# Kernel optimization log

Hardware: AMD Instinct MI355X
Metric: run time of the kernel (lower is better)

## Reference

```python
import jax, jax.numpy as jnp
import numpy as np

KH = KW = 3
SH = SW = 1
PH = PW = 1


def _im2col(x, kh, kw, sh, sw, ph, pw):
    # x: [N, C, H, W] -> cols: [N, C*kh*kw, H_out*W_out], ordering (C, kh, kw)
    N, C, H, W = x.shape
    H_out = (H + 2 * ph - kh) // sh + 1
    W_out = (W + 2 * pw - kw) // sw + 1
    x_pad = jnp.pad(x, ((0, 0), (0, 0), (ph, ph), (pw, pw)))
    # fixed small loop over kernel offsets (kh*kw = 9), strided slices
    patches = [x_pad[:, :, i:i + sh * H_out:sh, j:j + sw * W_out:sw]
               for i in range(kh) for j in range(kw)]  # each [N, C, H_out, W_out]
    cols = jnp.stack(patches, axis=2)  # [N, C, kh*kw, H_out, W_out]
    cols = cols.reshape(N, C * kh * kw, H_out * W_out)
    return cols, H_out, W_out


def setup_inputs() -> dict:
    key = jax.random.key(0)
    k1, k2, k3 = jax.random.split(key, 3)
    x = jax.random.normal(k1, (16, 128, 56, 56), dtype=jnp.float32)
    weight = jax.random.normal(k2, (256, 128, 3, 3), dtype=jnp.float32) * 0.05
    fan_in = 128 * 3 * 3
    bound = 1.0 / fan_in ** 0.5
    bias = jax.random.uniform(k3, (256,), dtype=jnp.float32, minval=-bound, maxval=bound)
    return {"x": x, "weight": weight, "bias": bias}


def reference(x, weight, bias):
    # im2col unfold + (analog) matmul conv; noise_cfg=None -> plain matmul
    cols, H_out, W_out = _im2col(x, KH, KW, SH, SW, PH, PW)  # [N, K, L]
    N = cols.shape[0]
    Cout = weight.shape[0]
    Wmat = weight.reshape(Cout, -1)  # [Cout, K], K = C*kh*kw
    # y[n, l, o] = sum_k cols[n, k, l] * Wmat[o, k]  (AnalogMatMulFn without noise)
    y = jnp.einsum('nkl,ok->nol', cols, Wmat)  # [N, Cout, L]
    y = y.reshape(N, Cout, H_out, W_out)
    y = y + bias[None, :, None, None]
    return y
```

## Files before the change

### kernel.cpp

```cpp
#include <hip/hip_runtime.h>
#include <hip/hip_bf16.h>
#include <stdint.h>


typedef __attribute__((ext_vector_type(8))) short short8;
typedef __attribute__((ext_vector_type(4))) float floatx4;

__device__ static inline void gload_lds16(const void* g, void* l) {
  typedef const __attribute__((address_space(1))) unsigned int* gp_t;
  typedef __attribute__((address_space(3))) unsigned int* lp_t;
  __builtin_amdgcn_global_load_lds((gp_t)(uintptr_t)g, (lp_t)(uint32_t)(uintptr_t)l,
                                   16, 0, 0);
}

__global__ __launch_bounds__(256)
void pre_kernel(const float* __restrict__ x, const float* __restrict__ wsrc,
                __hip_bfloat16* __restrict__ xp, __hip_bfloat16* __restrict__ wt) {
  const int b = blockIdx.x;
  if (b < 16 * 58) {
    const int n = b / 58, hp = b % 58;
    __hip_bfloat16* dst = xp + (size_t)(n * 58 + hp) * 58 * 128;
    if (hp == 0 || hp == 57) {
      const uint4 z = {0, 0, 0, 0};
      uint4* p = (uint4*)dst;
      for (int i = threadIdx.x; i < 928; i += 256) p[i] = z;
      return;
    }
    const int h = hp - 1;
    __shared__ float tile[128][57];
    const float* src = x + (size_t)n * (128 * 3136) + h * 56;
    for (int i = threadIdx.x; i < 128 * 14; i += 256) {
      const int c = i / 14, q = i - c * 14;
      const float4 v = ((const float4*)(src + (size_t)c * 3136))[q];
      tile[c][4 * q + 0] = v.x;
      tile[c][4 * q + 1] = v.y;
      tile[c][4 * q + 2] = v.z;
      tile[c][4 * q + 3] = v.w;
    }
    __syncthreads();
    if (threadIdx.x < 32) {
      const uint4 z = {0, 0, 0, 0};
      const int col = (threadIdx.x >> 4) * 57;
      ((uint4*)(dst + (size_t)col * 128))[threadIdx.x & 15] = z;
    }
    __hip_bfloat16* di = dst + 128;
    for (int i = threadIdx.x; i < 56 * 16; i += 256) {
      const int w = i >> 4, c8 = (i & 15) * 8;
      union { uint4 u; __hip_bfloat16 hh[8]; } pk;
#pragma unroll
      for (int j = 0; j < 8; ++j) pk.hh[j] = __float2bfloat16(tile[c8 + j][w]);
      *(uint4*)(di + (size_t)w * 128 + c8) = pk.u;
    }
  } else {
    const int base = (b - 928) * 256 + threadIdx.x;
    for (int t = base; t < 256 * 9 * 128; t += 36 * 256) {
      const int e = t & 7;
      const int rr = (t >> 3) & 15;
      const int q = (t >> 7) & 3;
      const int ks = (t >> 9) & 1;
      const int ch = (t >> 10) & 1;
      const int t11 = t >> 11;
      const int kq = t11 % 9;
      const int g = t11 / 9;
      const int cout = g * 16 + rr;
      const int c = ch * 64 + ks * 32 + q * 8 + e;
      wt[t] = __float2bfloat16(wsrc[(size_t)(cout * 128 + c) * 9 + kq]);
    }
  }
}

#define STAGE(PH, BUF)                                                        \
  {                                                                           \
    const char* _src = pbase + (PH) * (58 * 256);                             \
    _Pragma("unroll") for (int _i = 0; _i < 4; ++_i) {                        \
      const int _j = _i * 256 + tid;                                          \
      const int _row = _j >> 4;                                               \
      const int _slot = _j & 15;                                              \
      gload_lds16(_src + _row * 256 + ((_slot ^ (_row & 7)) << 4),            \
                  (BUF) + _i * 4096 + wave * 1024);                           \
    }                                                                         \
    if (wave == 0) {                                                          \
      const int _j = 1024 + lane;                                             \
      const int _row = _j >> 4;                                               \
      const int _slot = _j & 15;                                              \
      gload_lds16(_src + _row * 256 + ((_slot ^ (_row & 7)) << 4),            \
                  (BUF) + 16384);                                             \
    }                                                                         \
  }

#define COMPUTE(P, BUF)                                                       \
  _Pragma("clang loop unroll(disable)") for (int _t = 0; _t < 12; ++_t) {     \
    const int _kw = _t >> 2;                                                  \
    const int _ksl = _t & 3;                                                  \
    const int _ofs = (P) * 3 * 4096 + _kw * 4096 + _ksl * 1024;               \
    _Pragma("unroll") for (int _mt = 0; _mt < 4; ++_mt)                       \
        areg[_mt] = *(const short8*)(pAw + _mt * 36864 + _ofs);               \
    _Pragma("unroll") for (int _nt = 0; _nt < 4; ++_nt) {                     \
      const int _rowL = rbase[_nt] + _kw;                                     \
      const int _pos = (_ksl * 4 + quad) ^ (_rowL & 7);                       \
      bfr[_nt] = *(const short8*)((BUF) + _rowL * 256 + (_pos << 4));         \
    }                                                                         \
    _Pragma("unroll") for (int _mt = 0; _mt < 4; ++_mt)                       \
        _Pragma("unroll") for (int _nt = 0; _nt < 4; ++_nt)                   \
            acc[_mt][_nt] = __builtin_amdgcn_mfma_f32_16x16x32_bf16(          \
                areg[_mt], bfr[_nt], acc[_mt][_nt], 0, 0, 0);                 \
  }

__global__ __launch_bounds__(256, 4)
void conv_gemm_kernel(const __hip_bfloat16* __restrict__ xp,
                      const __hip_bfloat16* __restrict__ wt,
                      const float* __restrict__ bias,
                      float* __restrict__ out) {
  __shared__ __align__(16) char smem[2][17408];

  const int tid = threadIdx.x;
  const int lane = tid & 63;
  const int wave = tid >> 6;
  const int col = lane & 15;
  const int quad = lane >> 4;

  const int id = blockIdx.x;
  const int xcd = id & 7;
  const int nt_ = xcd * 98 + (id >> 3);
  const int n0 = nt_ * 64;

  const int nimg0 = n0 / 3136;
  const int rem0 = n0 - nimg0 * 3136;
  const int hh0 = rem0 / 56;
  const int ww0 = rem0 - hh0 * 56;
  const int P0 = (nimg0 * 58 + hh0) * 58 + ww0;
  const char* pbase = (const char*)xp + (size_t)P0 * 256;

  STAGE(0, smem[0]);

  const char* pAw = (const char*)wt + (size_t)(wave * 4) * 36864 + lane * 16;

  int rbase[4];
#pragma unroll
  for (int nt = 0; nt < 4; ++nt) {
    const int pix = n0 + nt * 16 + col;
    const int ni = pix / 3136;
    const int re = pix - ni * 3136;
    const int ph = re / 56;
    const int pw = re - ph * 56;
    rbase[nt] = (ni * 58 + ph) * 58 + pw - P0;
  }

  floatx4 acc[4][4];
#pragma unroll
  for (int a = 0; a < 4; ++a)
#pragma unroll
    for (int c = 0; c < 4; ++c) acc[a][c] = (floatx4)0.f;

  short8 areg[4], bfr[4];

  __syncthreads();
  STAGE(1, smem[1]);
  COMPUTE(0, smem[0]);
  __syncthreads();
  STAGE(2, smem[0]);
  COMPUTE(1, smem[1]);
  __syncthreads();
  COMPUTE(2, smem[0]);

  const int rb = quad * 4;
#pragma unroll
  for (int nt = 0; nt < 4; ++nt) {
    const int pix = n0 + nt * 16 + col;
    const int nimg = pix / 3136;
    const int rem = pix - nimg * 3136;
    float* op = out + (size_t)nimg * (256 * 3136) + rem;
#pragma unroll
    for (int mt = 0; mt < 4; ++mt) {
      const int mb = wave * 64 + mt * 16 + rb;
#pragma unroll
      for (int rr = 0; rr < 4; ++rr) {
        op[(size_t)(mb + rr) * 3136] = acc[mt][nt][rr] + bias[mb + rr];
      }
    }
  }
}

__global__ __launch_bounds__(256)
void direct_conv_kernel(const float* __restrict__ x, const float* __restrict__ wgt,
                        const float* __restrict__ bias, float* __restrict__ out) {
  const long t = (long)blockIdx.x * 256 + threadIdx.x;
  if (t >= 16L * 256 * 3136) return;
  const int w = t % 56;
  const int h = (t / 56) % 56;
  const int o = (t / 3136) % 256;
  const int n = t / (256L * 3136);
  float s = bias[o];
  for (int c = 0; c < 128; ++c)
    for (int kh = 0; kh < 3; ++kh) {
      const int hh = h + kh - 1;
      if (hh < 0 || hh >= 56) continue;
      for (int kw = 0; kw < 3; ++kw) {
        const int ww = w + kw - 1;
        if (ww < 0 || ww >= 56) continue;
        s += x[((size_t)(n * 128 + c) * 56 + hh) * 56 + ww] *
             wgt[((size_t)(o * 128 + c) * 3 + kh) * 3 + kw];
      }
    }
  out[t] = s;
}

extern "C" void kernel_launch(void* const* d_in, const int* in_sizes, int n_in,
                              void* d_out, int out_size, void* d_ws, size_t ws_size,
                              hipStream_t stream) {
  const float* x = (const float*)d_in[0];
  const float* w = (const float*)d_in[1];
  const float* b = (const float*)d_in[2];
  float* out = (float*)d_out;

  const size_t xp_bytes = (size_t)16 * 58 * 58 * 128 * 2;
  const size_t wt_bytes = (size_t)256 * 9 * 128 * 2;

  if (ws_size >= xp_bytes + wt_bytes) {
    __hip_bfloat16* xp = (__hip_bfloat16*)d_ws;
    __hip_bfloat16* wt = (__hip_bfloat16*)((char*)d_ws + xp_bytes);
    hipLaunchKernelGGL(pre_kernel, dim3(16 * 58 + 36), dim3(256), 0, stream,
                       x, w, xp, wt);
    hipLaunchKernelGGL(conv_gemm_kernel, dim3(784), dim3(256), 0, stream,
                       xp, wt, b, out);
  } else {
    const long total = 16L * 256 * 3136;
    hipLaunchKernelGGL(direct_conv_kernel, dim3((unsigned)((total + 255) / 256)),
                       dim3(256), 0, stream, x, w, b, out);
  }
}
```

Measured before the change: 126.7 us.

## Double pixel tile per block to 128 with 8 waves sharing staged input rows

The conv GEMM block grows from 256 to 512 threads and covers 128 output pixels instead of 64. Four waves split Cout and two split the pixels. Tiles are now aligned per image (25 tiles per image, the last one half-empty and masked), which removes the cross-image pixel math. This cuts the redundant halo loads of the 3-row input window per output pixel and halves the grid. In exchange it doubles LDS per block, wastes compute on tail tiles, and leaves fewer blocks (400) to fill the CUs.

```diff
diff --git a/kernel.cpp b/kernel.cpp
--- a/kernel.cpp
+++ b/kernel.cpp
@@ -73,18 +73,18 @@
   {                                                                           \
     const char* _src = pbase + (PH) * (58 * 256);                             \
     _Pragma("unroll") for (int _i = 0; _i < 4; ++_i) {                        \
-      const int _j = _i * 256 + tid;                                          \
+      const int _j = _i * 512 + tid;                                          \
       const int _row = _j >> 4;                                               \
       const int _slot = _j & 15;                                              \
       gload_lds16(_src + _row * 256 + ((_slot ^ (_row & 7)) << 4),            \
-                  (BUF) + _i * 4096 + wave * 1024);                           \
+                  (BUF) + _i * 8192 + wave * 1024);                           \
     }                                                                         \
-    if (wave == 0) {                                                          \
-      const int _j = 1024 + lane;                                             \
+    if (wave < 2) {                                                           \
+      const int _j = 2048 + wave * 64 + lane;                                 \
       const int _row = _j >> 4;                                               \
       const int _slot = _j & 15;                                              \
       gload_lds16(_src + _row * 256 + ((_slot ^ (_row & 7)) << 4),            \
-                  (BUF) + 16384);                                             \
+                  (BUF) + 32768 + wave * 1024);                               \
     }                                                                         \
   }
 
@@ -106,44 +106,48 @@
                 areg[_mt], bfr[_nt], acc[_mt][_nt], 0, 0, 0);                 \
   }
 
-__global__ __launch_bounds__(256, 4)
+__global__ __launch_bounds__(512, 4)
 void conv_gemm_kernel(const __hip_bfloat16* __restrict__ xp,
                       const __hip_bfloat16* __restrict__ wt,
                       const float* __restrict__ bias,
                       float* __restrict__ out) {
-  __shared__ __align__(16) char smem[2][17408];
+  __shared__ __align__(16) char smem[2][34816];
 
   const int tid = threadIdx.x;
   const int lane = tid & 63;
   const int wave = tid >> 6;
+  const int wm = wave & 3;
+  const int wn = wave >> 2;
   const int col = lane & 15;
   const int quad = lane >> 4;
 
   const int id = blockIdx.x;
-  const int xcd = id & 7;
-  const int nt_ = xcd * 98 + (id >> 3);
-  const int n0 = nt_ * 64;
-
-  const int nimg0 = n0 / 3136;
-  const int rem0 = n0 - nimg0 * 3136;
+  const int g = (id & 7) * 50 + (id >> 3);
+  const int img = g / 25;
+  const int t = g - img * 25;
+  const int n0 = img * 3136 + t * 128;
+  const bool tail = (t == 24);
+  const int pmax = img * 3136 + 3135;
+
+  const int rem0 = n0 - img * 3136;
   const int hh0 = rem0 / 56;
   const int ww0 = rem0 - hh0 * 56;
-  const int P0 = (nimg0 * 58 + hh0) * 58 + ww0;
+  const int P0 = (img * 58 + hh0) * 58 + ww0;
   const char* pbase = (const char*)xp + (size_t)P0 * 256;
 
   STAGE(0, smem[0]);
 
-  const char* pAw = (const char*)wt + (size_t)(wave * 4) * 36864 + lane * 16;
+  const char* pAw = (const char*)wt + (size_t)(wm * 4) * 36864 + lane * 16;
 
   int rbase[4];
 #pragma unroll
   for (int nt = 0; nt < 4; ++nt) {
-    const int pix = n0 + nt * 16 + col;
-    const int ni = pix / 3136;
-    const int re = pix - ni * 3136;
+    int pix = n0 + wn * 64 + nt * 16 + col;
+    if (pix > pmax) pix = pmax;
+    const int re = pix - img * 3136;
     const int ph = re / 56;
     const int pw = re - ph * 56;
-    rbase[nt] = (ni * 58 + ph) * 58 + pw - P0;
+    rbase[nt] = (ph - hh0) * 58 + (pw - ww0);
   }
 
   floatx4 acc[4][4];
@@ -163,19 +167,20 @@
   __syncthreads();
   COMPUTE(2, smem[0]);
 
-  const int rb = quad * 4;
-#pragma unroll
-  for (int nt = 0; nt < 4; ++nt) {
-    const int pix = n0 + nt * 16 + col;
-    const int nimg = pix / 3136;
-    const int rem = pix - nimg * 3136;
-    float* op = out + (size_t)nimg * (256 * 3136) + rem;
-#pragma unroll
-    for (int mt = 0; mt < 4; ++mt) {
-      const int mb = wave * 64 + mt * 16 + rb;
-#pragma unroll
-      for (int rr = 0; rr < 4; ++rr) {
-        op[(size_t)(mb + rr) * 3136] = acc[mt][nt][rr] + bias[mb + rr];
+  if (!(tail && wn)) {
+    const int rb = quad * 4;
+#pragma unroll
+    for (int nt = 0; nt < 4; ++nt) {
+      const int pix = n0 + wn * 64 + nt * 16 + col;
+      const int rem = pix - img * 3136;
+      float* op = out + (size_t)img * (256 * 3136) + rem;
+#pragma unroll
+      for (int mt = 0; mt < 4; ++mt) {
+        const int mb = wm * 64 + mt * 16 + rb;
+#pragma unroll
+        for (int rr = 0; rr < 4; ++rr) {
+          op[(size_t)(mb + rr) * 3136] = acc[mt][nt][rr] + bias[mb + rr];
+        }
       }
     }
   }
@@ -221,7 +226,7 @@
     __hip_bfloat16* wt = (__hip_bfloat16*)((char*)d_ws + xp_bytes);
     hipLaunchKernelGGL(pre_kernel, dim3(16 * 58 + 36), dim3(256), 0, stream,
                        x, w, xp, wt);
-    hipLaunchKernelGGL(conv_gemm_kernel, dim3(784), dim3(256), 0, stream,
+    hipLaunchKernelGGL(conv_gemm_kernel, dim3(400), dim3(512), 0, stream,
                        xp, wt, b, out);
   } else {
     const long total = 16L * 256 * 3136;
```

Measured after the change: 131.1 us. +3.5%, slower.

## Double-buffer weight fragments in registers with async asm loads and manual vmcnt

Applied to the files above, without the earlier changes.

Weight (A) fragments are now loaded with inline-asm global_load_dwordx4 into two alternating register sets. The next k-step's weights are prefetched while the current MFMAs run, and explicit s_waitcnt vmcnt(4) waits plus a sched_barrier gate the consumption. The goal is to hide global-load latency of the weight operand, which previously was loaded and then immediately consumed each step. The extra registers lead to lowering the launch-bounds occupancy hint from 4 to 3 blocks. There is a risk that the manual vmcnt counting interacts with the in-flight global_load_lds staging loads and forces extra waits.

```diff
diff --git a/kernel.cpp b/kernel.cpp
--- a/kernel.cpp
+++ b/kernel.cpp
@@ -88,25 +88,43 @@
     }                                                                         \
   }
 
-#define COMPUTE(P, BUF)                                                       \
-  _Pragma("clang loop unroll(disable)") for (int _t = 0; _t < 12; ++_t) {     \
+#define ALOAD(DST, VOFF)                                                      \
+  asm volatile("global_load_dwordx4 %0, %1, %2"                               \
+               : "=v"(DST) : "v"(VOFF), "s"(wtb64) : "memory")
+
+#define HALF_STEP(SET, T, BUF, LASTWAIT, SKIP)                                \
+  {                                                                           \
+    const int _t = (T);                                                       \
     const int _kw = _t >> 2;                                                  \
     const int _ksl = _t & 3;                                                  \
-    const int _ofs = (P) * 3 * 4096 + _kw * 4096 + _ksl * 1024;               \
-    _Pragma("unroll") for (int _mt = 0; _mt < 4; ++_mt)                       \
-        areg[_mt] = *(const short8*)(pAw + _mt * 36864 + _ofs);               \
     _Pragma("unroll") for (int _nt = 0; _nt < 4; ++_nt) {                     \
       const int _rowL = rbase[_nt] + _kw;                                     \
       const int _pos = (_ksl * 4 + quad) ^ (_rowL & 7);                       \
       bfr[_nt] = *(const short8*)((BUF) + _rowL * 256 + (_pos << 4));         \
     }                                                                         \
+    if (LASTWAIT) { asm volatile("s_waitcnt vmcnt(0)" ::: "memory"); }        \
+    else          { asm volatile("s_waitcnt vmcnt(4)" ::: "memory"); }        \
+    __builtin_amdgcn_sched_barrier(0);                                        \
     _Pragma("unroll") for (int _mt = 0; _mt < 4; ++_mt)                       \
         _Pragma("unroll") for (int _nt = 0; _nt < 4; ++_nt)                   \
             acc[_mt][_nt] = __builtin_amdgcn_mfma_f32_16x16x32_bf16(          \
-                areg[_mt], bfr[_nt], acc[_mt][_nt], 0, 0, 0);                 \
-  }
-
-__global__ __launch_bounds__(256, 4)
+                SET[_mt], bfr[_nt], acc[_mt][_nt], 0, 0, 0);                  \
+    if (!(SKIP)) {                                                            \
+      _Pragma("unroll") for (int _mt = 0; _mt < 4; ++_mt) {                   \
+        ALOAD(SET[_mt], voff[_mt]);                                           \
+        voff[_mt] += 1024;                                                    \
+      }                                                                       \
+    }                                                                         \
+  }
+
+#define COMPUTE_PH(P, BUF, LASTP)                                             \
+  _Pragma("clang loop unroll(disable)") for (int _dd = 0; _dd < 6; ++_dd) {   \
+    HALF_STEP(aregP, 2 * _dd, BUF, false, (LASTP) && _dd == 5)                \
+    HALF_STEP(aregQ, 2 * _dd + 1, BUF, (LASTP) && _dd == 5,                   \
+              (LASTP) && _dd == 5)                                            \
+  }
+
+__global__ __launch_bounds__(256, 3)
 void conv_gemm_kernel(const __hip_bfloat16* __restrict__ xp,
                       const __hip_bfloat16* __restrict__ wt,
                       const float* __restrict__ bias,
@@ -133,7 +151,19 @@
 
   STAGE(0, smem[0]);
 
-  const char* pAw = (const char*)wt + (size_t)(wave * 4) * 36864 + lane * 16;
+  const uint64_t wtb64 = (uint64_t)(uintptr_t)wt;
+
+  uint32_t voff[4];
+#pragma unroll
+  for (int mt = 0; mt < 4; ++mt)
+    voff[mt] = (uint32_t)((wave * 4 + mt) * 36864 + lane * 16);
+
+  short8 aregP[4], aregQ[4], bfr[4];
+
+#pragma unroll
+  for (int mt = 0; mt < 4; ++mt) { ALOAD(aregP[mt], voff[mt]); voff[mt] += 1024; }
+#pragma unroll
+  for (int mt = 0; mt < 4; ++mt) { ALOAD(aregQ[mt], voff[mt]); voff[mt] += 1024; }
 
   int rbase[4];
 #pragma unroll
@@ -152,16 +182,14 @@
 #pragma unroll
     for (int c = 0; c < 4; ++c) acc[a][c] = (floatx4)0.f;
 
-  short8 areg[4], bfr[4];
-
   __syncthreads();
   STAGE(1, smem[1]);
-  COMPUTE(0, smem[0]);
+  COMPUTE_PH(0, smem[0], false);
   __syncthreads();
   STAGE(2, smem[0]);
-  COMPUTE(1, smem[1]);
+  COMPUTE_PH(1, smem[1], false);
   __syncthreads();
-  COMPUTE(2, smem[0]);
+  COMPUTE_PH(2, smem[0], true);
 
   const int rb = quad * 4;
 #pragma unroll
```

Result: faster. 122.2 us (-3.6%).
